# Performance work log

Hardware: AMD Instinct MI355X
Metric: run time of the kernel (lower is better)

The kernel has to match this reference:

```python
import jax, jax.numpy as jnp
import numpy as np

B, N, E, K, DI, DO = 16, 1024, 16, 3, 32, 32


def setup_inputs() -> dict:
    key = jax.random.key(0)
    k1, k2, k3, k4, k5 = jax.random.split(key, 5)
    return {
        "x": jax.random.normal(k1, (B, N, DI), dtype=jnp.float32),
        "all_emb": jax.random.normal(k2, (B, N, E), dtype=jnp.float32),
        "stock_emb": jax.random.normal(k3, (B, N, E), dtype=jnp.float32),
        "weights_pool": jax.random.normal(k4, (E, K, DI, DO), dtype=jnp.float32) * 0.1,
        "bias_pool": jax.random.normal(k5, (E, DO), dtype=jnp.float32) * 0.1,
    }


def reference(x, all_emb, stock_emb, weights_pool, bias_pool):
    # dynamic adjacency: relu(E E^T) then row softmax -> [B, N, N]
    A = jax.nn.relu(jnp.einsum('bne,bme->bnm', all_emb, all_emb))
    S = jax.nn.softmax(A, axis=-1)
    b, n, _ = S.shape
    k_orders = weights_pool.shape[1]
    eye = jnp.broadcast_to(jnp.eye(n, dtype=S.dtype), S.shape)
    # Chebyshev recursion T_0 = I, T_1 = S, T_k = 2 S T_{k-1} - T_{k-2}
    supports = [eye, S]
    for _ in range(2, k_orders):
        supports.append(2.0 * jnp.matmul(S, supports[-1]) - supports[-2])
    cheby = jnp.stack(supports, axis=1)  # [B, K, N, N]
    # graph propagation per Chebyshev order: [B, K, N, dim_in]
    x_g = jnp.einsum('bkij,bjd->bkid', cheby, x)
    # node-specific weights from stock_emb, fused with conv (avoids [B,N,K,I,O]):
    # original: weights = einsum('bni,ikop->bnkop'); out = einsum('bkni,bnkio->bnko').sum(k)
    out = jnp.einsum('bkni,bne,ekio->bno', x_g, stock_emb, weights_pool)
    bias = jnp.einsum('bne,eo->bno', stock_emb, bias_pool)
    return out + bias
```

## Files before the change

### kernel.cpp

```cpp
#include <hip/hip_runtime.h>
#include <stdint.h>

typedef __bf16 bf16x8 __attribute__((ext_vector_type(8)));
typedef __bf16 bf16x4 __attribute__((ext_vector_type(4)));
typedef float  f32x16 __attribute__((ext_vector_type(16)));

constexpr int kB = 16;
constexpr int kN = 1024;
constexpr float kLog2e = 1.44269504088896340736f;

struct bfhl { __bf16 h, l; };
__device__ __forceinline__ bfhl hilo(float v) {
    bfhl r;
    r.h = (__bf16)v;
    r.l = (__bf16)(v - (float)r.h);
    return r;
}

__device__ __forceinline__ int moff(int f, int h, int j) {
    return 16 * f + ((j < 4) ? (4 * h + j) : (4 * h + j + 4));
}


__global__ __launch_bounds__(256) void prep(
    const float* __restrict__ emb, const float* __restrict__ x,
    const float* __restrict__ Wp,
    __bf16* __restrict__ esf, __bf16* __restrict__ esq,
    __bf16* __restrict__ vtf1, __bf16* __restrict__ wq)
{
    __shared__ float ls[64 * 36];
    const int tid = threadIdx.x;
    const int bid = blockIdx.x;

    if (bid < 256) {
        const int b = bid >> 4, rg = (bid & 15) << 6;
        const int r = tid >> 2, seg = tid & 3;
        float4 v = *(const float4*)(emb + ((size_t)(b * kN + rg + r) * 16 + seg * 4));
        float f[4] = {v.x, v.y, v.z, v.w};
        bf16x4 hi, lo, qhi, qlo;
        #pragma unroll
        for (int i = 0; i < 4; ++i) {
            bfhl t = hilo(f[i]);           hi[i] = t.h;  lo[i] = t.l;
            bfhl s = hilo(f[i] * kLog2e);  qhi[i] = s.h; qlo[i] = s.l;
        }
        const int kt = ((bid & 15) << 1) + (r >> 5);
        const int lane = ((seg >> 1) << 5) + (r & 31);
        const int j0 = (seg & 1) << 2;
        const size_t off = ((size_t)(b * 32 + kt) * 2) * 512 + lane * 8 + j0;
        *(bf16x4*)(esf + off)       = hi;
        *(bf16x4*)(esf + off + 512) = lo;
        *(bf16x4*)(esq + off)       = qhi;
        *(bf16x4*)(esq + off + 512) = qlo;
    } else if (bid < 512) {
        const int bb = bid - 256;
        const int b = bb >> 4, n0 = (bb & 15) << 6;
        const float* sB = x + ((size_t)b * kN + n0) * 32;
        #pragma unroll
        for (int it = 0; it < 2; ++it) {
            int f = it * 256 + tid;
            int row = f >> 3, q8 = f & 7;
            float4 v = *(const float4*)(sB + (size_t)row * 32 + q8 * 4);
            *(float4*)(&ls[row * 36 + q8 * 4]) = v;
        }
        __syncthreads();
        {
            const int mt = tid >> 7, fr = (tid >> 6) & 1, l = tid & 63;
            const int d = l & 31, h = l >> 5;
            bf16x8 ov;
            #pragma unroll
            for (int j = 0; j < 8; ++j)
                ov[j] = (__bf16)ls[(mt * 32 + moff(fr, h, j)) * 36 + d];
            *(bf16x8*)(vtf1 + ((size_t)(b * 32 + (n0 >> 5) + mt) * 2 + fr) * 512 + l * 8) = ov;
        }
    } else {
        int idx = (bid - 512) * 256 + tid;
        if (idx < 6144) {
            int e = idx / 384, rem = idx - e * 384;
            int ks = rem / 64, r2 = rem - ks * 64;
            int o = r2 >> 1, hh = r2 & 1;
            int ki0 = ks * 16 + hh * 8;
            bf16x8 hi;
            #pragma unroll
            for (int j = 0; j < 8; ++j)
                hi[j] = (__bf16)Wp[(size_t)e * 3072 + (size_t)(ki0 + j) * 32 + o];
            *(bf16x8*)(wq + (size_t)(e * 6 + ks) * 512 + o * 16 + hh * 8) = hi;
        }
    }
}

template<int STAGE>
__global__ __launch_bounds__(256, 2) void apply_mfma(
    const __bf16* __restrict__ esf, const __bf16* __restrict__ esq,
    const __bf16* __restrict__ vtin,
    const float*  __restrict__ x,
    __bf16* __restrict__ vtout, __bf16* __restrict__ y1f,
    const __bf16* __restrict__ wq,
    const float*  __restrict__ stock, const float* __restrict__ bias,
    float* __restrict__ out)
{
    __shared__ alignas(16) char smem[28672];
    float*  ps  = (float*)smem;
    float*  Ls  = (float*)(smem + 16896);
    float*  yb  = (float*)(smem + 17408);
    __bf16* xg2 = (__bf16*)(smem + 22016);
    float*  s_s = (float*)(smem + 26624);

    const int tid = threadIdx.x;
    const int w = tid >> 6, l = tid & 63;
    const int q = l & 31, h = l >> 5;
    const int bs = ((blockIdx.x & 7) << 6) | (blockIdx.x >> 3);
    const int b = bs >> 5, nt = bs & 31, q0 = nt << 5;
    const int gnt = b * 32 + nt;

    const __bf16* esfB = esf + (size_t)b * 32768;
    const __bf16* esqB = esq + (size_t)b * 32768;
    const __bf16* vtfB = vtin + (size_t)b * 32768;

    if (STAGE == 2) {
        int r = tid >> 3, e2 = (tid & 7) * 2;
        *(float2*)(s_s + r * 16 + e2) =
            *(const float2*)(stock + (size_t)(b * kN + q0 + r) * 16 + e2);
    }

    bf16x8 bhi = *(const bf16x8*)(esqB + ((size_t)nt * 2) * 512 + l * 8);
    bf16x8 blo = *(const bf16x8*)(esqB + ((size_t)nt * 2 + 1) * 512 + l * 8);

    f32x16 acc = {};
    float Lp = 0.f;

#define LOADK(kt, ahi, alo, V0, V1) \
    ahi = *(const bf16x8*)(esfB + ((size_t)(kt) * 2) * 512 + l * 8);     \
    alo = *(const bf16x8*)(esfB + ((size_t)(kt) * 2 + 1) * 512 + l * 8); \
    V0  = *(const bf16x8*)(vtfB + ((size_t)(kt) * 2) * 512 + l * 8);     \
    V1  = *(const bf16x8*)(vtfB + ((size_t)(kt) * 2 + 1) * 512 + l * 8);

    const int ktb = w * 8;
    bf16x8 cahiA, caloA, cV0A, cV1A, cahiB, caloB, cV0B, cV1B;
    LOADK(ktb + 0, cahiA, caloA, cV0A, cV1A);
    LOADK(ktb + 1, cahiB, caloB, cV0B, cV1B);

    #pragma unroll
    for (int it = 0; it < 4; ++it) {
        bf16x8 nahiA, naloA, nV0A, nV1A, nahiB, naloB, nV0B, nV1B;
        if (it < 3) {
            LOADK(ktb + it * 2 + 2, nahiA, naloA, nV0A, nV1A);
            LOADK(ktb + it * 2 + 3, nahiB, naloB, nV0B, nV1B);
        }
        f32x16 S0 = {}, S1 = {};
        S0 = __builtin_amdgcn_mfma_f32_32x32x16_bf16(cahiA, bhi, S0, 0, 0, 0);
        S1 = __builtin_amdgcn_mfma_f32_32x32x16_bf16(cahiB, bhi, S1, 0, 0, 0);
        S0 = __builtin_amdgcn_mfma_f32_32x32x16_bf16(cahiA, blo, S0, 0, 0, 0);
        S1 = __builtin_amdgcn_mfma_f32_32x32x16_bf16(cahiB, blo, S1, 0, 0, 0);
        S0 = __builtin_amdgcn_mfma_f32_32x32x16_bf16(caloA, bhi, S0, 0, 0, 0);
        S1 = __builtin_amdgcn_mfma_f32_32x32x16_bf16(caloB, bhi, S1, 0, 0, 0);

        float p0[16], p1[16];
        #pragma unroll
        for (int r = 0; r < 16; ++r) {
            p0[r] = exp2f(fmaxf(S0[r], 0.f));  Lp += p0[r];
            p1[r] = exp2f(fmaxf(S1[r], 0.f));  Lp += p1[r];
        }
        bf16x8 P00, P01, P10, P11;
        #pragma unroll
        for (int j = 0; j < 8; ++j) {
            P00[j] = (__bf16)p0[j]; P01[j] = (__bf16)p0[8 + j];
            P10[j] = (__bf16)p1[j]; P11[j] = (__bf16)p1[8 + j];
        }
        acc = __builtin_amdgcn_mfma_f32_32x32x16_bf16(cV0A, P00, acc, 0, 0, 0);
        acc = __builtin_amdgcn_mfma_f32_32x32x16_bf16(cV1A, P01, acc, 0, 0, 0);
        acc = __builtin_amdgcn_mfma_f32_32x32x16_bf16(cV0B, P10, acc, 0, 0, 0);
        acc = __builtin_amdgcn_mfma_f32_32x32x16_bf16(cV1B, P11, acc, 0, 0, 0);

        cahiA = nahiA; caloA = naloA; cV0A = nV0A; cV1A = nV1A;
        cahiB = nahiB; caloB = naloB; cV0B = nV0B; cV1B = nV1B;
    }
#undef LOADK

    Lp += __shfl_xor(Lp, 32);
    #pragma unroll
    for (int r = 0; r < 16; ++r) {
        int d = (r & 3) + 8 * (r >> 2) + 4 * h;
        ps[w * 1056 + d * 33 + q] = acc[r];
    }
    if (l < 32) Ls[w * 32 + l] = Lp;
    __syncthreads();

    const int qq = tid >> 3, dg = tid & 7;
    const float iL = 1.f / (Ls[qq] + Ls[32 + qq] + Ls[64 + qq] + Ls[96 + qq]);
    float yv[4];
    #pragma unroll
    for (int i = 0; i < 4; ++i) {
        int d = dg * 4 + i;
        yv[i] = (ps[d * 33 + qq] + ps[1056 + d * 33 + qq] +
                 ps[2112 + d * 33 + qq] + ps[3168 + d * 33 + qq]) * iL;
    }

    if (STAGE == 1) {
        #pragma unroll
        for (int i = 0; i < 4; ++i) yb[qq * 36 + dg * 4 + i] = yv[i];
        __syncthreads();
        if (tid < 128) {
            int fr = tid >> 6, l2 = tid & 63;
            int d = l2 & 31, h2 = l2 >> 5;
            bf16x8 ov;
            #pragma unroll
            for (int j = 0; j < 8; ++j)
                ov[j] = (__bf16)yb[moff(fr, h2, j) * 36 + d];
            *(bf16x8*)(vtout + ((size_t)gnt * 2 + fr) * 512 + l2 * 8) = ov;
        }
        {
            int ks2 = tid >> 7, pl = (tid >> 6) & 1, l2 = tid & 63;
            int node = l2 & 31, h2 = l2 >> 5;
            const float* rp = yb + node * 36 + ks2 * 16 + 8 * h2;
            bf16x8 ov;
            #pragma unroll
            for (int j = 0; j < 8; ++j) {
                bfhl tt = hilo(rp[j]);
                ov[j] = pl ? tt.l : tt.h;
            }
            *(bf16x8*)(y1f + (((size_t)gnt * 2 + ks2) * 2 + pl) * 512 + l2 * 8) = ov;
        }
    } else {
        {
            float4 xv = *(const float4*)(x + (size_t)(b * kN + q0 + qq) * 32 + dg * 4);
            float xa[4] = {xv.x, xv.y, xv.z, xv.w};
            bf16x4 hi, lo;
            #pragma unroll
            for (int i = 0; i < 4; ++i) {
                bfhl tt = hilo(2.f * yv[i] - xa[i]);
                hi[i] = tt.h; lo[i] = tt.l;
            }
            *(bf16x4*)(xg2 + qq * 36 + dg * 4)        = hi;
            *(bf16x4*)(xg2 + 1152 + qq * 36 + dg * 4) = lo;
        }
        __syncthreads();

        f32x16 acc2[4] = {};
        const int e0 = w * 4;
        const int o = q;

        #pragma unroll
        for (int ks = 0; ks < 6; ++ks) {
            bf16x8 Ah, Al;
            if (ks < 2) {
                const float* rp = x + (size_t)(b * kN + q0 + q) * 32 + ks * 16 + 8 * h;
                float4 u0 = *(const float4*)rp;
                float4 u1 = *(const float4*)(rp + 4);
                float u[8] = {u0.x, u0.y, u0.z, u0.w, u1.x, u1.y, u1.z, u1.w};
                #pragma unroll
                for (int j = 0; j < 8; ++j) { bfhl tt = hilo(u[j]); Ah[j] = tt.h; Al[j] = tt.l; }
            } else if (ks < 4) {
                Ah = *(const bf16x8*)(y1f + (((size_t)gnt * 2 + (ks - 2)) * 2 + 0) * 512 + l * 8);
                Al = *(const bf16x8*)(y1f + (((size_t)gnt * 2 + (ks - 2)) * 2 + 1) * 512 + l * 8);
            } else {
                const int base = o * 36 + (ks - 4) * 16 + 8 * h;
                bf16x4 a0 = *(const bf16x4*)(xg2 + base);
                bf16x4 a1 = *(const bf16x4*)(xg2 + base + 4);
                bf16x4 b0 = *(const bf16x4*)(xg2 + 1152 + base);
                bf16x4 b1 = *(const bf16x4*)(xg2 + 1152 + base + 4);
                #pragma unroll
                for (int j = 0; j < 4; ++j) {
                    Ah[j] = a0[j]; Ah[4 + j] = a1[j];
                    Al[j] = b0[j]; Al[4 + j] = b1[j];
                }
            }
            #pragma unroll
            for (int ei = 0; ei < 4; ++ei) {
                bf16x8 Bh = *(const bf16x8*)(wq + (size_t)((e0 + ei) * 6 + ks) * 512 + o * 16 + h * 8);
                acc2[ei] = __builtin_amdgcn_mfma_f32_32x32x16_bf16(Ah, Bh, acc2[ei], 0, 0, 0);
                acc2[ei] = __builtin_amdgcn_mfma_f32_32x32x16_bf16(Al, Bh, acc2[ei], 0, 0, 0);
            }
        }

        float pr[16];
        #pragma unroll
        for (int r = 0; r < 16; ++r) pr[r] = 0.f;
        #pragma unroll
        for (int ei = 0; ei < 4; ++ei) {
            const int eg = e0 + ei;
            const float bv = bias[eg * 32 + o];
            #pragma unroll
            for (int r = 0; r < 16; ++r) {
                int node = (r & 3) + 8 * (r >> 2) + 4 * h;
                pr[r] += s_s[node * 16 + eg] * (acc2[ei][r] + bv);
            }
        }
        #pragma unroll
        for (int r = 0; r < 16; ++r) {
            int node = (r & 3) + 8 * (r >> 2) + 4 * h;
            ps[w * 1056 + node * 33 + o] = pr[r];
        }
        __syncthreads();
        {
            const int node = tid >> 3, og = (tid & 7) * 4;
            float4 s;
            #pragma unroll
            for (int i = 0; i < 4; ++i) {
                int c = node * 33 + og + i;
                ((float*)&s)[i] = ps[c] + ps[1056 + c] + ps[2112 + c] + ps[3168 + c];
            }
            *(float4*)(out + (size_t)(b * kN + q0 + node) * 32 + og) = s;
        }
    }
}

extern "C" void kernel_launch(void* const* d_in, const int* in_sizes, int n_in,
                              void* d_out, int out_size, void* d_ws, size_t ws_size,
                              hipStream_t stream) {
    const float* x     = (const float*)d_in[0];
    const float* aemb  = (const float*)d_in[1];
    const float* stock = (const float*)d_in[2];
    const float* Wp    = (const float*)d_in[3];
    const float* bias  = (const float*)d_in[4];
    float* out = (float*)d_out;

    __bf16* wsb  = (__bf16*)d_ws;
    __bf16* esf  = wsb;
    __bf16* esq  = wsb + 524288;
    __bf16* vtf1 = wsb + 1048576;
    __bf16* vtf2 = wsb + 1572864;
    __bf16* y1f  = wsb + 2097152;
    __bf16* wq   = wsb + 3145728;

    prep<<<dim3(536), dim3(256), 0, stream>>>(aemb, x, Wp, esf, esq, vtf1, wq);
    apply_mfma<1><<<dim3(512), dim3(256), 0, stream>>>(
        esf, esq, vtf1, x, vtf2, y1f, wq, stock, bias, out);
    apply_mfma<2><<<dim3(512), dim3(256), 0, stream>>>(
        esf, esq, vtf2, x, nullptr, y1f, wq, stock, bias, out);
}
```

Before: 28.95 us.

## Fold prep kernel into apply stages, converting embeddings and x on the fly

```diff
diff --git a/kernel.cpp b/kernel.cpp
--- a/kernel.cpp
+++ b/kernel.cpp
@@ -21,81 +21,15 @@
     return 16 * f + ((j < 4) ? (4 * h + j) : (4 * h + j + 4));
 }
 
-
-__global__ __launch_bounds__(256) void prep(
+template<int STAGE>
+__global__ __launch_bounds__(256, 2) void apply_mfma(
     const float* __restrict__ emb, const float* __restrict__ x,
     const float* __restrict__ Wp,
-    __bf16* __restrict__ esf, __bf16* __restrict__ esq,
-    __bf16* __restrict__ vtf1, __bf16* __restrict__ wq)
-{
-    __shared__ float ls[64 * 36];
-    const int tid = threadIdx.x;
-    const int bid = blockIdx.x;
-
-    if (bid < 256) {
-        const int b = bid >> 4, rg = (bid & 15) << 6;
-        const int r = tid >> 2, seg = tid & 3;
-        float4 v = *(const float4*)(emb + ((size_t)(b * kN + rg + r) * 16 + seg * 4));
-        float f[4] = {v.x, v.y, v.z, v.w};
-        bf16x4 hi, lo, qhi, qlo;
-        #pragma unroll
-        for (int i = 0; i < 4; ++i) {
-            bfhl t = hilo(f[i]);           hi[i] = t.h;  lo[i] = t.l;
-            bfhl s = hilo(f[i] * kLog2e);  qhi[i] = s.h; qlo[i] = s.l;
-        }
-        const int kt = ((bid & 15) << 1) + (r >> 5);
-        const int lane = ((seg >> 1) << 5) + (r & 31);
-        const int j0 = (seg & 1) << 2;
-        const size_t off = ((size_t)(b * 32 + kt) * 2) * 512 + lane * 8 + j0;
-        *(bf16x4*)(esf + off)       = hi;
-        *(bf16x4*)(esf + off + 512) = lo;
-        *(bf16x4*)(esq + off)       = qhi;
-        *(bf16x4*)(esq + off + 512) = qlo;
-    } else if (bid < 512) {
-        const int bb = bid - 256;
-        const int b = bb >> 4, n0 = (bb & 15) << 6;
-        const float* sB = x + ((size_t)b * kN + n0) * 32;
-        #pragma unroll
-        for (int it = 0; it < 2; ++it) {
-            int f = it * 256 + tid;
-            int row = f >> 3, q8 = f & 7;
-            float4 v = *(const float4*)(sB + (size_t)row * 32 + q8 * 4);
-            *(float4*)(&ls[row * 36 + q8 * 4]) = v;
-        }
-        __syncthreads();
-        {
-            const int mt = tid >> 7, fr = (tid >> 6) & 1, l = tid & 63;
-            const int d = l & 31, h = l >> 5;
-            bf16x8 ov;
-            #pragma unroll
-            for (int j = 0; j < 8; ++j)
-                ov[j] = (__bf16)ls[(mt * 32 + moff(fr, h, j)) * 36 + d];
-            *(bf16x8*)(vtf1 + ((size_t)(b * 32 + (n0 >> 5) + mt) * 2 + fr) * 512 + l * 8) = ov;
-        }
-    } else {
-        int idx = (bid - 512) * 256 + tid;
-        if (idx < 6144) {
-            int e = idx / 384, rem = idx - e * 384;
-            int ks = rem / 64, r2 = rem - ks * 64;
-            int o = r2 >> 1, hh = r2 & 1;
-            int ki0 = ks * 16 + hh * 8;
-            bf16x8 hi;
-            #pragma unroll
-            for (int j = 0; j < 8; ++j)
-                hi[j] = (__bf16)Wp[(size_t)e * 3072 + (size_t)(ki0 + j) * 32 + o];
-            *(bf16x8*)(wq + (size_t)(e * 6 + ks) * 512 + o * 16 + hh * 8) = hi;
-        }
-    }
-}
-
-template<int STAGE>
-__global__ __launch_bounds__(256, 2) void apply_mfma(
-    const __bf16* __restrict__ esf, const __bf16* __restrict__ esq,
+    const float* __restrict__ stock, const float* __restrict__ bias,
     const __bf16* __restrict__ vtin,
-    const float*  __restrict__ x,
-    __bf16* __restrict__ vtout, __bf16* __restrict__ y1f,
-    const __bf16* __restrict__ wq,
-    const float*  __restrict__ stock, const float* __restrict__ bias,
+    __bf16* __restrict__ vtout,
+    __bf16* __restrict__ y1f,
+    __bf16* __restrict__ wq,
     float* __restrict__ out)
 {
     __shared__ alignas(16) char smem[28672];
@@ -112,69 +46,122 @@
     const int b = bs >> 5, nt = bs & 31, q0 = nt << 5;
     const int gnt = b * 32 + nt;
 
-    const __bf16* esfB = esf + (size_t)b * 32768;
-    const __bf16* esqB = esq + (size_t)b * 32768;
-    const __bf16* vtfB = vtin + (size_t)b * 32768;
-
+    const float* embB = emb + (size_t)b * kN * 16;
+    const float* xB   = x + (size_t)b * kN * 32;
+    const __bf16* vtinB = vtin + (size_t)b * 32768;
+
+    if (STAGE == 1) {
+        if (blockIdx.x < 48 && tid < 128) {
+            int idx = blockIdx.x * 128 + tid;
+            int e = idx / 384, rem = idx - e * 384;
+            int ks = rem / 64, r2 = rem - ks * 64;
+            int o = r2 >> 1, hh = r2 & 1;
+            int ki0 = ks * 16 + hh * 8;
+            bf16x8 hi;
+            #pragma unroll
+            for (int j = 0; j < 8; ++j)
+                hi[j] = (__bf16)Wp[(size_t)e * 3072 + (size_t)(ki0 + j) * 32 + o];
+            *(bf16x8*)(wq + (size_t)(e * 6 + ks) * 512 + o * 16 + hh * 8) = hi;
+        }
+    }
     if (STAGE == 2) {
         int r = tid >> 3, e2 = (tid & 7) * 2;
         *(float2*)(s_s + r * 16 + e2) =
             *(const float2*)(stock + (size_t)(b * kN + q0 + r) * 16 + e2);
     }
 
-    bf16x8 bhi = *(const bf16x8*)(esqB + ((size_t)nt * 2) * 512 + l * 8);
-    bf16x8 blo = *(const bf16x8*)(esqB + ((size_t)nt * 2 + 1) * 512 + l * 8);
+    bf16x8 bhi, blo;
+    {
+        const float* ep = embB + (size_t)(q0 + q) * 16 + 8 * h;
+        float4 u0 = *(const float4*)ep;
+        float4 u1 = *(const float4*)(ep + 4);
+        float u[8] = {u0.x, u0.y, u0.z, u0.w, u1.x, u1.y, u1.z, u1.w};
+        #pragma unroll
+        for (int j = 0; j < 8; ++j) {
+            bfhl t = hilo(u[j] * kLog2e);
+            bhi[j] = t.h; blo[j] = t.l;
+        }
+    }
 
     f32x16 acc = {};
     float Lp = 0.f;
 
-#define LOADK(kt, ahi, alo, V0, V1) \
-    ahi = *(const bf16x8*)(esfB + ((size_t)(kt) * 2) * 512 + l * 8);     \
-    alo = *(const bf16x8*)(esfB + ((size_t)(kt) * 2 + 1) * 512 + l * 8); \
-    V0  = *(const bf16x8*)(vtfB + ((size_t)(kt) * 2) * 512 + l * 8);     \
-    V1  = *(const bf16x8*)(vtfB + ((size_t)(kt) * 2 + 1) * 512 + l * 8);
-
-    const int ktb = w * 8;
-    bf16x8 cahiA, caloA, cV0A, cV1A, cahiB, caloB, cV0B, cV1B;
-    LOADK(ktb + 0, cahiA, caloA, cV0A, cV1A);
-    LOADK(ktb + 1, cahiB, caloB, cV0B, cV1B);
-
-    #pragma unroll
-    for (int it = 0; it < 4; ++it) {
-        bf16x8 nahiA, naloA, nV0A, nV1A, nahiB, naloB, nV0B, nV1B;
-        if (it < 3) {
-            LOADK(ktb + it * 2 + 2, nahiA, naloA, nV0A, nV1A);
-            LOADK(ktb + it * 2 + 3, nahiB, naloB, nV0B, nV1B);
-        }
-        f32x16 S0 = {}, S1 = {};
-        S0 = __builtin_amdgcn_mfma_f32_32x32x16_bf16(cahiA, bhi, S0, 0, 0, 0);
-        S1 = __builtin_amdgcn_mfma_f32_32x32x16_bf16(cahiB, bhi, S1, 0, 0, 0);
-        S0 = __builtin_amdgcn_mfma_f32_32x32x16_bf16(cahiA, blo, S0, 0, 0, 0);
-        S1 = __builtin_amdgcn_mfma_f32_32x32x16_bf16(cahiB, blo, S1, 0, 0, 0);
-        S0 = __builtin_amdgcn_mfma_f32_32x32x16_bf16(caloA, bhi, S0, 0, 0, 0);
-        S1 = __builtin_amdgcn_mfma_f32_32x32x16_bf16(caloB, bhi, S1, 0, 0, 0);
-
-        float p0[16], p1[16];
-        #pragma unroll
-        for (int r = 0; r < 16; ++r) {
-            p0[r] = exp2f(fmaxf(S0[r], 0.f));  Lp += p0[r];
-            p1[r] = exp2f(fmaxf(S1[r], 0.f));  Lp += p1[r];
-        }
-        bf16x8 P00, P01, P10, P11;
-        #pragma unroll
-        for (int j = 0; j < 8; ++j) {
-            P00[j] = (__bf16)p0[j]; P01[j] = (__bf16)p0[8 + j];
-            P10[j] = (__bf16)p1[j]; P11[j] = (__bf16)p1[8 + j];
-        }
-        acc = __builtin_amdgcn_mfma_f32_32x32x16_bf16(cV0A, P00, acc, 0, 0, 0);
-        acc = __builtin_amdgcn_mfma_f32_32x32x16_bf16(cV1A, P01, acc, 0, 0, 0);
-        acc = __builtin_amdgcn_mfma_f32_32x32x16_bf16(cV0B, P10, acc, 0, 0, 0);
-        acc = __builtin_amdgcn_mfma_f32_32x32x16_bf16(cV1B, P11, acc, 0, 0, 0);
-
-        cahiA = nahiA; caloA = naloA; cV0A = nV0A; cV1A = nV1A;
-        cahiB = nahiB; caloB = naloB; cV0B = nV0B; cV1B = nV1B;
-    }
-#undef LOADK
+#define LOADE(kt_, e0_, e1_) {                                            \
+    const float* ep_ = embB + (size_t)((kt_) * 32 + q) * 16 + 8 * h;      \
+    e0_ = *(const float4*)ep_; e1_ = *(const float4*)(ep_ + 4); }
+#define LOADV1(kt_, vv_) {                                                \
+    _Pragma("unroll")                                                     \
+    for (int j_ = 0; j_ < 8; ++j_) {                                      \
+        vv_[j_]     = xB[(size_t)((kt_) * 32 + moff(0, h, j_)) * 32 + q]; \
+        vv_[8 + j_] = xB[(size_t)((kt_) * 32 + moff(1, h, j_)) * 32 + q]; } }
+#define LOADV2(kt_, A0_, A1_) {                                           \
+    A0_ = *(const bf16x8*)(vtinB + ((size_t)(kt_) * 2) * 512 + l * 8);    \
+    A1_ = *(const bf16x8*)(vtinB + ((size_t)(kt_) * 2 + 1) * 512 + l * 8); }
+
+    {
+        const int ktb = w * 8;
+        float4 e0c, e1c, e0n, e1n;
+        float vc[16], vn[16];
+        bf16x8 A0c, A1c, A0n, A1n;
+
+        LOADE(ktb, e0c, e1c);
+        if (STAGE == 1) { LOADV1(ktb, vc) } else { LOADV2(ktb, A0c, A1c) }
+
+        #pragma unroll
+        for (int it = 0; it < 8; ++it) {
+            if (it < 7) {
+                LOADE(ktb + it + 1, e0n, e1n);
+                if (STAGE == 1) { LOADV1(ktb + it + 1, vn) }
+                else            { LOADV2(ktb + it + 1, A0n, A1n) }
+            }
+            float ef[8] = {e0c.x, e0c.y, e0c.z, e0c.w, e1c.x, e1c.y, e1c.z, e1c.w};
+            bf16x8 ahi, alo;
+            #pragma unroll
+            for (int j = 0; j < 8; ++j) {
+                bfhl t = hilo(ef[j]);
+                ahi[j] = t.h; alo[j] = t.l;
+            }
+            bf16x8 A0, A1;
+            if (STAGE == 1) {
+                #pragma unroll
+                for (int j = 0; j < 8; ++j) {
+                    A0[j] = (__bf16)vc[j];
+                    A1[j] = (__bf16)vc[8 + j];
+                }
+            } else { A0 = A0c; A1 = A1c; }
+
+            __builtin_amdgcn_s_setprio(1);
+            f32x16 S = {};
+            S = __builtin_amdgcn_mfma_f32_32x32x16_bf16(ahi, bhi, S, 0, 0, 0);
+            S = __builtin_amdgcn_mfma_f32_32x32x16_bf16(ahi, blo, S, 0, 0, 0);
+            S = __builtin_amdgcn_mfma_f32_32x32x16_bf16(alo, bhi, S, 0, 0, 0);
+            __builtin_amdgcn_s_setprio(0);
+
+            float p[16];
+            #pragma unroll
+            for (int r = 0; r < 16; ++r) {
+                p[r] = exp2f(fmaxf(S[r], 0.f));
+                Lp += p[r];
+            }
+            bf16x8 P0, P1;
+            #pragma unroll
+            for (int j = 0; j < 8; ++j) { P0[j] = (__bf16)p[j]; P1[j] = (__bf16)p[8 + j]; }
+
+            __builtin_amdgcn_s_setprio(1);
+            acc = __builtin_amdgcn_mfma_f32_32x32x16_bf16(A0, P0, acc, 0, 0, 0);
+            acc = __builtin_amdgcn_mfma_f32_32x32x16_bf16(A1, P1, acc, 0, 0, 0);
+            __builtin_amdgcn_s_setprio(0);
+
+            e0c = e0n; e1c = e1n;
+            if (STAGE == 1) {
+                #pragma unroll
+                for (int j = 0; j < 16; ++j) vc[j] = vn[j];
+            } else { A0c = A0n; A1c = A1n; }
+        }
+    }
+#undef LOADE
+#undef LOADV1
+#undef LOADV2
 
     Lp += __shfl_xor(Lp, 32);
     #pragma unroll
@@ -222,7 +209,7 @@
         }
     } else {
         {
-            float4 xv = *(const float4*)(x + (size_t)(b * kN + q0 + qq) * 32 + dg * 4);
+            float4 xv = *(const float4*)(xB + (size_t)(q0 + qq) * 32 + dg * 4);
             float xa[4] = {xv.x, xv.y, xv.z, xv.w};
             bf16x4 hi, lo;
             #pragma unroll
@@ -243,7 +230,7 @@
         for (int ks = 0; ks < 6; ++ks) {
             bf16x8 Ah, Al;
             if (ks < 2) {
-                const float* rp = x + (size_t)(b * kN + q0 + q) * 32 + ks * 16 + 8 * h;
+                const float* rp = xB + (size_t)(q0 + q) * 32 + ks * 16 + 8 * h;
                 float4 u0 = *(const float4*)rp;
                 float4 u1 = *(const float4*)(rp + 4);
                 float u[8] = {u0.x, u0.y, u0.z, u0.w, u1.x, u1.y, u1.z, u1.w};
@@ -315,16 +302,12 @@
     float* out = (float*)d_out;
 
     __bf16* wsb  = (__bf16*)d_ws;
-    __bf16* esf  = wsb;
-    __bf16* esq  = wsb + 524288;
-    __bf16* vtf1 = wsb + 1048576;
-    __bf16* vtf2 = wsb + 1572864;
-    __bf16* y1f  = wsb + 2097152;
-    __bf16* wq   = wsb + 3145728;
-
-    prep<<<dim3(536), dim3(256), 0, stream>>>(aemb, x, Wp, esf, esq, vtf1, wq);
+    __bf16* vtf2 = wsb;
+    __bf16* y1f  = wsb + 524288;
+    __bf16* wq   = wsb + 1572864;
+
     apply_mfma<1><<<dim3(512), dim3(256), 0, stream>>>(
-        esf, esq, vtf1, x, vtf2, y1f, wq, stock, bias, out);
+        aemb, x, Wp, stock, bias, nullptr, vtf2, y1f, wq, out);
     apply_mfma<2><<<dim3(512), dim3(256), 0, stream>>>(
-        esf, esq, vtf2, x, nullptr, y1f, wq, stock, bias, out);
+        aemb, x, Wp, stock, bias, vtf2, nullptr, y1f, wq, out);
 }
```

Measured after the change: 29.00 us. Within noise of the previous version (+0.2%).
